# Kernel optimization log

Hardware: AMD Instinct MI355X
Metric: run time of the kernel (lower is better)

## Reference

```python
import jax, jax.numpy as jnp
import numpy as np

B, S, F_IN, D, H, DFF, L = 64, 256, 64, 512, 8, 2048, 6
A_DIM, FEAT, OUT = 8, 32, 5
EPS = 1e-3  # keras default epsilon for BatchNorm/LayerNorm


def _sinusoidal_pes(seq_len, d_model):
    pos = np.arange(seq_len)[:, None].astype(np.float32)
    i = np.arange(d_model)[None, :].astype(np.float32)
    angle = pos / np.power(10000.0, (2.0 * np.floor(i / 2.0)) / d_model)
    pe = np.zeros((seq_len, d_model), dtype=np.float32)
    pe[:, 0::2] = np.sin(angle[:, 0::2])
    pe[:, 1::2] = np.cos(angle[:, 1::2])
    return jnp.asarray(pe)


def setup_inputs() -> dict:
    key = jax.random.key(0)
    ks = jax.random.split(key, 16)
    w = lambda k, shape: 0.02 * jax.random.normal(k, shape, dtype=jnp.float32)
    return {
        'state': jax.random.normal(ks[0], (B, S, F_IN), dtype=jnp.float32),
        'action': jax.random.normal(ks[1], (B, A_DIM), dtype=jnp.float32),
        'pes': _sinusoidal_pes(S, D),
        'W_emb': w(ks[2], (F_IN, D)), 'b_emb': jnp.zeros((D,), jnp.float32),
        'Wq': w(ks[3], (L, D, D)), 'bq': jnp.zeros((L, D), jnp.float32),
        'Wk': w(ks[4], (L, D, D)), 'bk': jnp.zeros((L, D), jnp.float32),
        'Wv': w(ks[5], (L, D, D)), 'bv': jnp.zeros((L, D), jnp.float32),
        'Wo': w(ks[6], (L, D, D)), 'bo': jnp.zeros((L, D), jnp.float32),
        'bn_gamma': jnp.ones((L, D), jnp.float32), 'bn_beta': jnp.zeros((L, D), jnp.float32),
        'W1': w(ks[7], (L, D, DFF)), 'b1': jnp.zeros((L, DFF), jnp.float32),
        'W2': w(ks[8], (L, DFF, D)), 'b2': jnp.zeros((L, D), jnp.float32),
        'ln_gamma': jnp.ones((L, D), jnp.float32), 'ln_beta': jnp.zeros((L, D), jnp.float32),
        'Wf': w(ks[9], (S * D, FEAT)), 'bf': jnp.zeros((FEAT,), jnp.float32),
        'Wfin': w(ks[10], (FEAT + A_DIM, OUT)), 'bfin': jnp.zeros((OUT,), jnp.float32),
    }


def _encoder(x, pes, layer_params):
    # x: [B, S, D]
    x = x + pes  # positional encoding

    def step(h, p):
        Wq, bq, Wk, bk, Wv, bv, Wo, bo, gb, bb, W1, b1, W2, b2, gl, bl = p
        b, s, d = h.shape
        dh = d // H
        q = (h @ Wq + bq).reshape(b, s, H, dh)
        k = (h @ Wk + bk).reshape(b, s, H, dh)
        v = (h @ Wv + bv).reshape(b, s, H, dh)
        scores = jnp.einsum('bqhd,bkhd->bhqk', q, k) / jnp.sqrt(jnp.asarray(dh, h.dtype))
        attn = jax.nn.softmax(scores, axis=-1)
        ctx = jnp.einsum('bhqk,bkhd->bqhd', attn, v).reshape(b, s, d)
        ctx = ctx @ Wo + bo
        y = h + ctx
        # BatchNormalization over (batch, seq), per-channel (training-mode batch stats)
        mu = y.mean(axis=(0, 1))
        var = y.var(axis=(0, 1))
        y = gb * (y - mu) * jax.lax.rsqrt(var + EPS) + bb
        # FFN + residual + LayerNorm
        f = jax.nn.relu(y @ W1 + b1) @ W2 + b2
        z = y + f
        mu2 = z.mean(axis=-1, keepdims=True)
        var2 = z.var(axis=-1, keepdims=True)
        z = gl * (z - mu2) * jax.lax.rsqrt(var2 + EPS) + bl
        return z, None

    x, _ = jax.lax.scan(step, x, layer_params)
    return x


def reference(state, action, pes, W_emb, b_emb, Wq, bq, Wk, bk, Wv, bv, Wo, bo,
              bn_gamma, bn_beta, W1, b1, W2, b2, ln_gamma, ln_beta, Wf, bf, Wfin, bfin):
    x = state @ W_emb + b_emb                       # [B, S, D]
    layer_params = (Wq, bq, Wk, bk, Wv, bv, Wo, bo, bn_gamma, bn_beta,
                    W1, b1, W2, b2, ln_gamma, ln_beta)
    enc = _encoder(x, pes, layer_params)            # [B, S, D]
    flat = enc.reshape(enc.shape[0], -1)            # [B, S*D]
    feat = flat @ Wf + bf                           # [B, 32]
    out = jnp.concatenate([feat, action], axis=-1) @ Wfin + bfin  # [B, 5]
    return out
```

## Files before the change

kernel.cpp:

```cpp
#include <hip/hip_runtime.h>

typedef short bf16x8 __attribute__((ext_vector_type(8)));
typedef float f32x4 __attribute__((ext_vector_type(4)));
typedef unsigned short us;

#define BN_EPS 1e-3f

static __device__ __forceinline__ us f2bs(float x) {
  unsigned int u = __builtin_bit_cast(unsigned int, x);
  unsigned int r = (u + 0x7FFFu + ((u >> 16) & 1u)) >> 16;
  return (us)r;
}
static __device__ __forceinline__ float b2f(us v) {
  unsigned int u = (unsigned int)v << 16;
  return __builtin_bit_cast(float, u);
}

static __device__ __forceinline__ void gl_lds16(const us* g, us* l) {
  __builtin_amdgcn_global_load_lds(
      (const __attribute__((address_space(1))) void*)g,
      (__attribute__((address_space(3))) void*)l, 16, 0, 0);
}

__global__ __launch_bounds__(256) void transpose_bf16(
    const float* __restrict__ src, us* __restrict__ dst, int K, int N,
    long sstride, long dstride) {
  long sbs = (long)blockIdx.z * sstride;
  long sbd = (long)blockIdx.z * dstride;
  __shared__ float tile[32][33];
  int tx = threadIdx.x & 31, ty = threadIdx.x >> 5;
  int k0 = blockIdx.x * 32, n0 = blockIdx.y * 32;
  for (int i = 0; i < 32; i += 8)
    tile[ty + i][tx] = src[sbs + (long)(k0 + ty + i) * N + n0 + tx];
  __syncthreads();
  for (int i = 0; i < 32; i += 8)
    dst[sbd + (long)(n0 + ty + i) * K + k0 + tx] = f2bs(tile[tx][ty + i]);
}

__global__ __launch_bounds__(256) void embed_kernel(
    const float* __restrict__ state, const float* __restrict__ Wemb,
    const float* __restrict__ bemb, const float* __restrict__ pes,
    us* __restrict__ hb) {
  int t = threadIdx.x;
  int row0 = blockIdx.x * 8;
  __shared__ float st[8][64];
  {
    int i = t;
    st[i >> 6][i & 63] = state[(long)row0 * 64 + i];
    i += 256;
    st[i >> 6][i & 63] = state[(long)row0 * 64 + i];
  }
  __syncthreads();
  int c0 = t, c1 = t + 256;
  float acc0[8], acc1[8];
#pragma unroll
  for (int r = 0; r < 8; ++r) { acc0[r] = 0.f; acc1[r] = 0.f; }
  for (int kk = 0; kk < 64; ++kk) {
    float w0 = Wemb[kk * 512 + c0], w1 = Wemb[kk * 512 + c1];
#pragma unroll
    for (int r = 0; r < 8; ++r) {
      acc0[r] += st[r][kk] * w0;
      acc1[r] += st[r][kk] * w1;
    }
  }
  float be0 = bemb[c0], be1 = bemb[c1];
#pragma unroll
  for (int r = 0; r < 8; ++r) {
    int row = row0 + r, s = row & 255;
    hb[(long)row * 512 + c0] = f2bs(acc0[r] + be0 + pes[(long)s * 512 + c0]);
    hb[(long)row * 512 + c1] = f2bs(acc1[r] + be1 + pes[(long)s * 512 + c1]);
  }
}

enum { EPI_QKV = 0, EPI_RESID_BF16 = 1, EPI_RELU_BF16 = 2, EPI_FFN2_F32 = 3,
       EPI_FEAT = 4 };

template <int BM, int BN, int WM, int WN, int EPI>
__global__ __launch_bounds__((BM / WM) * (BN / WN) * 64)
void gemm_bt(const us* __restrict__ A, int lda, long batchA,
             const us* __restrict__ Bt, int ldb, long batchB,
             void* __restrict__ Cout, void* __restrict__ C2,
             void* __restrict__ C3, int ldc,
             const float* __restrict__ bias,
             const us* __restrict__ resid,
             const float* __restrict__ gsum, const float* __restrict__ gsumsq,
             const float* __restrict__ gamma, const float* __restrict__ beta,
             int K) {
  constexpr int WCols = BN / WN;
  constexpr int NT = (BM / WM) * (BN / WN) * 64;
  constexpr int NW = NT / 64;
  constexpr int MI = WM / 16, NI = WN / 16;
  constexpr int LA = BM / 8;
  constexpr int LB = BN / 8;
  const int tid = threadIdx.x;
  const int w = tid >> 6, l = tid & 63;
  const int wr = w / WCols, wc = w % WCols;
  const int lr = l & 15, lh = l >> 4;
  const int z = blockIdx.z;
  const long m0 = (long)blockIdx.x * BM;
  const long n0 = (long)blockIdx.y * BN;
  A += (long)z * batchA;
  Bt += (long)z * batchB;
  __shared__ __align__(16) us smem[BM * 64 + BN * 64];
  us* Asm = smem;
  us* Bsm = smem + BM * 64;
  const int srow = l >> 3, scol = (l & 7) << 3;
  f32x4 acc[MI][NI] = {};
  for (int kt = 0; kt < K; kt += 64) {
    __syncthreads();
    for (int j = w; j < LA; j += NW) {
      int rb = j * 8;
      gl_lds16(A + (m0 + rb + srow) * lda + kt + scol, Asm + rb * 64);
    }
    for (int j = w; j < LB; j += NW) {
      int rb = j * 8;
      gl_lds16(Bt + (n0 + rb + srow) * ldb + kt + scol, Bsm + rb * 64);
    }
    asm volatile("s_waitcnt vmcnt(0)" ::: "memory");
    __syncthreads();
#pragma unroll
    for (int kk = 0; kk < 64; kk += 32) {
      bf16x8 af[MI], bfr[NI];
#pragma unroll
      for (int mi = 0; mi < MI; ++mi)
        af[mi] = *(const bf16x8*)&Asm[(wr * WM + mi * 16 + lr) * 64 + kk + lh * 8];
#pragma unroll
      for (int ni = 0; ni < NI; ++ni)
        bfr[ni] = *(const bf16x8*)&Bsm[(wc * WN + ni * 16 + lr) * 64 + kk + lh * 8];
#pragma unroll
      for (int mi = 0; mi < MI; ++mi)
#pragma unroll
        for (int ni = 0; ni < NI; ++ni)
          acc[mi][ni] = __builtin_amdgcn_mfma_f32_16x16x32_bf16(
              af[mi], bfr[ni], acc[mi][ni], 0, 0, 0);
    }
  }

  if constexpr (EPI == EPI_QKV) {
    const int seg = (int)(n0 >> 9);
    const int nc0 = (int)(n0 & 511);
    if (seg == 2) {
#pragma unroll
      for (int mi = 0; mi < MI; ++mi) {
#pragma unroll
        for (int ni = 0; ni < NI; ++ni) {
          const int segc = nc0 + wc * WN + ni * 16 + lr;
          const float bv_ = beta[segc];
          ushort4 pv;
#pragma unroll
          for (int q_ = 0; q_ < 4; ++q_)
            ((us*)&pv)[q_] = f2bs(acc[mi][ni][q_] + bv_);
          const long row0g = m0 + wr * WM + mi * 16 + lh * 4;
          const long o = (((row0g >> 8) * 8 + (segc >> 6)) * 64 + (segc & 63)) *
                             256 + (row0g & 255);
          *(ushort4*)&((us*)C3)[o] = pv;
        }
      }
    } else {
      __syncthreads();
#pragma unroll
      for (int mi = 0; mi < MI; ++mi)
#pragma unroll
        for (int ni = 0; ni < NI; ++ni) {
          const int cl = wc * WN + ni * 16 + lr;
          const float bv_ = seg == 0 ? bias[nc0 + cl] : gamma[nc0 + cl];
#pragma unroll
          for (int q_ = 0; q_ < 4; ++q_) {
            const int rl = wr * WM + mi * 16 + lh * 4 + q_;
            smem[rl * BN + cl] = f2bs(acc[mi][ni][q_] + bv_);
          }
        }
      __syncthreads();
      us* dstp = seg == 0 ? (us*)Cout : (us*)C2;
      for (int i = tid; i < (BM * BN) / 8; i += NT) {
        const int idx = i * 8;
        const int row = idx / BN, colc = idx % BN;
        *(uint4*)&dstp[(m0 + row) * 512 + nc0 + colc] = *(uint4*)&smem[idx];
      }
    }
  } else if constexpr ((EPI == EPI_RELU_BF16 || EPI == EPI_RESID_BF16) &&
                       BM == 128 && BN == 128) {
    __syncthreads();
#pragma unroll
    for (int mi = 0; mi < MI; ++mi)
#pragma unroll
      for (int ni = 0; ni < NI; ++ni) {
        const int cl = wc * WN + ni * 16 + lr;
        const float bv_ = bias[(int)n0 + cl];
#pragma unroll
        for (int q_ = 0; q_ < 4; ++q_) {
          const int rl = wr * WM + mi * 16 + lh * 4 + q_;
          float v = acc[mi][ni][q_] + bv_;
          if constexpr (EPI == EPI_RELU_BF16) {
            smem[rl * BN + cl] = f2bs(fmaxf(v, 0.f));
          } else {
            v += b2f(resid[(m0 + rl) * ldc + (int)n0 + cl]);
            smem[rl * BN + cl] = f2bs(v);
          }
        }
      }
    __syncthreads();
    for (int i = tid; i < (BM * BN) / 8; i += NT) {
      const int idx = i * 8;
      const int row = idx / BN, colc = idx % BN;
      *(uint4*)&((us*)Cout)[(m0 + row) * ldc + n0 + colc] = *(uint4*)&smem[idx];
    }
  } else {
#pragma unroll
    for (int mi = 0; mi < MI; ++mi) {
#pragma unroll
      for (int ni = 0; ni < NI; ++ni) {
        const int col = (int)n0 + wc * WN + ni * 16 + lr;
        float bv_ = 0.f;
        if constexpr (EPI != EPI_FEAT) bv_ = bias[col];
        float aa = 0.f, bb2 = 0.f;
        if constexpr (EPI == EPI_FFN2_F32) {
          const float invN = 1.f / 16384.f;
          float mu = gsum[col] * invN;
          float var = gsumsq[col] * invN - mu * mu;
          aa = gamma[col] * rsqrtf(var + BN_EPS);
          bb2 = beta[col] - mu * aa;
        }
#pragma unroll
        for (int q_ = 0; q_ < 4; ++q_) {
          const long row = m0 + wr * WM + mi * 16 + lh * 4 + q_;
          float v = acc[mi][ni][q_] + bv_;
          if constexpr (EPI == EPI_FEAT) {
            atomicAdd(&((float*)Cout)[row * ldc + col], v);
          } else if constexpr (EPI == EPI_FFN2_F32) {
            float ybn = b2f(resid[row * ldc + col]) * aa + bb2;
            ((float*)Cout)[row * ldc + col] = ybn + v;
          }
        }
      }
    }
  }
}

__global__ __launch_bounds__(256) void attn_kernel(
    const us* __restrict__ q, const us* __restrict__ k,
    const us* __restrict__ vt, us* __restrict__ ctx) {
  const int half = blockIdx.x;
  const int z = blockIdx.y;
  const int b = z >> 3, hh = z & 7;
  const long qkBase = (long)b * 131072 + hh * 64;
  const int tid = threadIdx.x, w = tid >> 6, l = tid & 63;
  const int lr = l & 15, lh = l >> 4;
  __shared__ __align__(16) us Qs[32][72];
  __shared__ __align__(16) us Ks[64][72];
  __shared__ __align__(16) us Pb[32][264];
  __shared__ float fred[32][2];
  const int qr = (w >> 1) * 16, qc = (w & 1) * 32;
  const us* vb = vt + (long)z * 16384;
  const int ldr = tid >> 3, ldc = (tid & 7) << 3;

  for (int qi = 0; qi < 4; ++qi) {
    const int qb = half * 4 + qi;
    *(uint4*)&Qs[ldr][ldc] =
        *(const uint4*)(q + qkBase + (long)(qb * 32 + ldr) * 512 + ldc);
    f32x4 sacc[4][2] = {};
    for (int skb = 0; skb < 4; ++skb) {
      __syncthreads();
      for (int i = tid; i < 512; i += 256) {
        int r = i >> 3, c = (i & 7) << 3;
        *(uint4*)&Ks[r][c] =
            *(const uint4*)(k + qkBase + (long)(skb * 64 + r) * 512 + c);
      }
      __syncthreads();
#pragma unroll
      for (int kh = 0; kh < 2; ++kh) {
        bf16x8 aq = *(const bf16x8*)&Qs[qr + lr][kh * 32 + lh * 8];
#pragma unroll
        for (int ni = 0; ni < 2; ++ni) {
          bf16x8 bkk = *(const bf16x8*)&Ks[qc + ni * 16 + lr][kh * 32 + lh * 8];
          sacc[skb][ni] = __builtin_amdgcn_mfma_f32_16x16x32_bf16(
              aq, bkk, sacc[skb][ni], 0, 0, 0);
        }
      }
    }
    float m0[4] = {-1e30f, -1e30f, -1e30f, -1e30f};
#pragma unroll
    for (int skb = 0; skb < 4; ++skb)
#pragma unroll
      for (int ni = 0; ni < 2; ++ni)
#pragma unroll
        for (int q_ = 0; q_ < 4; ++q_) {
          float v = sacc[skb][ni][q_] * 0.125f;
          sacc[skb][ni][q_] = v;
          m0[q_] = fmaxf(m0[q_], v);
        }
#pragma unroll
    for (int off = 1; off < 16; off <<= 1)
#pragma unroll
      for (int q_ = 0; q_ < 4; ++q_)
        m0[q_] = fmaxf(m0[q_], __shfl_xor(m0[q_], off));
    if (lr == 0) {
#pragma unroll
      for (int q_ = 0; q_ < 4; ++q_) fred[qr + lh * 4 + q_][w & 1] = m0[q_];
    }
    __syncthreads();
#pragma unroll
    for (int q_ = 0; q_ < 4; ++q_) {
      int row = qr + lh * 4 + q_;
      m0[q_] = fmaxf(fred[row][0], fred[row][1]);
    }
    float s0[4] = {0.f, 0.f, 0.f, 0.f};
#pragma unroll
    for (int skb = 0; skb < 4; ++skb)
#pragma unroll
      for (int ni = 0; ni < 2; ++ni)
#pragma unroll
        for (int q_ = 0; q_ < 4; ++q_) {
          float e = __expf(sacc[skb][ni][q_] - m0[q_]);
          sacc[skb][ni][q_] = e;
          s0[q_] += e;
        }
#pragma unroll
    for (int off = 1; off < 16; off <<= 1)
#pragma unroll
      for (int q_ = 0; q_ < 4; ++q_) s0[q_] += __shfl_xor(s0[q_], off);
    __syncthreads();
    if (lr == 0) {
#pragma unroll
      for (int q_ = 0; q_ < 4; ++q_) fred[qr + lh * 4 + q_][w & 1] = s0[q_];
    }
    __syncthreads();
#pragma unroll
    for (int q_ = 0; q_ < 4; ++q_) {
      int row = qr + lh * 4 + q_;
      s0[q_] = 1.f / (fred[row][0] + fred[row][1]);
    }
#pragma unroll
    for (int skb = 0; skb < 4; ++skb)
#pragma unroll
      for (int ni = 0; ni < 2; ++ni)
#pragma unroll
        for (int q_ = 0; q_ < 4; ++q_)
          Pb[qr + lh * 4 + q_][skb * 64 + qc + ni * 16 + lr] =
              f2bs(sacc[skb][ni][q_] * s0[q_]);
    f32x4 pacc[2] = {};
    for (int kc = 0; kc < 256; kc += 64) {
      __syncthreads();
      for (int i = tid; i < 512; i += 256) {
        int r = i >> 3, c = (i & 7) << 3;
        *(uint4*)&Ks[r][c] = *(const uint4*)(vb + (long)r * 256 + kc + c);
      }
      __syncthreads();
#pragma unroll
      for (int kh = 0; kh < 2; ++kh) {
        bf16x8 ap = *(const bf16x8*)&Pb[qr + lr][kc + kh * 32 + lh * 8];
#pragma unroll
        for (int ni = 0; ni < 2; ++ni) {
          bf16x8 bv2 = *(const bf16x8*)&Ks[qc + ni * 16 + lr][kh * 32 + lh * 8];
          pacc[ni] = __builtin_amdgcn_mfma_f32_16x16x32_bf16(
              ap, bv2, pacc[ni], 0, 0, 0);
        }
      }
    }
    const long cb2 = ((long)(b * 256 + qb * 32)) * 512 + hh * 64;
#pragma unroll
    for (int ni = 0; ni < 2; ++ni)
#pragma unroll
      for (int q_ = 0; q_ < 4; ++q_) {
        int row = qr + lh * 4 + q_;
        int col = qc + ni * 16 + lr;
        ctx[cb2 + (long)row * 512 + col] = f2bs(pacc[ni][q_]);
      }
  }
}

__global__ __launch_bounds__(256) void bn_stats(const us* __restrict__ y,
                                                float* __restrict__ gsum,
                                                float* __restrict__ gsumsq) {
  int t = threadIdx.x;
  long base = (long)blockIdx.x * 64 * 512;
  float s0 = 0, q0 = 0, s1 = 0, q1 = 0;
  for (int r = 0; r < 64; ++r) {
    ushort2 v = *(const ushort2*)(y + base + r * 512 + 2 * t);
    float v0 = b2f(v.x), v1 = b2f(v.y);
    s0 += v0; q0 += v0 * v0;
    s1 += v1; q1 += v1 * v1;
  }
  atomicAdd(&gsum[2 * t], s0);
  atomicAdd(&gsumsq[2 * t], q0);
  atomicAdd(&gsum[2 * t + 1], s1);
  atomicAdd(&gsumsq[2 * t + 1], q1);
}

__global__ __launch_bounds__(256) void bn_apply(
    const us* __restrict__ y, const float* __restrict__ gsum,
    const float* __restrict__ gsumsq, const float* __restrict__ gamma,
    const float* __restrict__ beta, us* __restrict__ ybb) {
  long e = ((long)blockIdx.x * 256 + threadIdx.x) * 4;
  int c = (int)(e & 511);
  const float invN = 1.f / 16384.f;
  ushort4 v = *(const ushort4*)(y + e);
  ushort4 r;
#pragma unroll
  for (int j = 0; j < 4; ++j) {
    int cj = c + j;
    float mu = gsum[cj] * invN;
    float var = gsumsq[cj] * invN - mu * mu;
    float a = gamma[cj] * rsqrtf(var + BN_EPS);
    float b = beta[cj] - mu * a;
    ((us*)&r)[j] = f2bs(b2f(((us*)&v)[j]) * a + b);
  }
  *(ushort4*)(ybb + e) = r;
}

__global__ __launch_bounds__(128) void ln_kernel(
    const float* __restrict__ zin, const float* __restrict__ g,
    const float* __restrict__ b, us* __restrict__ hb) {
  int r = blockIdx.x, t = threadIdx.x;
  const float* zr = zin + (long)r * 512;
  float4 v = *(const float4*)(zr + t * 4);
  float s = v.x + v.y + v.z + v.w;
  float qs = v.x * v.x + v.y * v.y + v.z * v.z + v.w * v.w;
  for (int off = 32; off >= 1; off >>= 1) {
    s += __shfl_down(s, off);
    qs += __shfl_down(qs, off);
  }
  __shared__ float ls[2], lq[2];
  if ((t & 63) == 0) {
    ls[t >> 6] = s;
    lq[t >> 6] = qs;
  }
  __syncthreads();
  float mu = (ls[0] + ls[1]) * (1.f / 512.f);
  float var = (lq[0] + lq[1]) * (1.f / 512.f) - mu * mu;
  float rs = rsqrtf(var + BN_EPS);
  float4 gg = *(const float4*)(g + t * 4);
  float4 bb = *(const float4*)(b + t * 4);
  ushort4 hv;
  ((us*)&hv)[0] = f2bs(gg.x * (v.x - mu) * rs + bb.x);
  ((us*)&hv)[1] = f2bs(gg.y * (v.y - mu) * rs + bb.y);
  ((us*)&hv)[2] = f2bs(gg.z * (v.z - mu) * rs + bb.z);
  ((us*)&hv)[3] = f2bs(gg.w * (v.w - mu) * rs + bb.w);
  *(ushort4*)(hb + (long)r * 512 + t * 4) = hv;
}

__global__ void zerof(float* __restrict__ p, int n) {
  int i = blockIdx.x * 256 + threadIdx.x;
  if (i < n) p[i] = 0.f;
}

__global__ __launch_bounds__(320) void final_head(
    const float* __restrict__ feat, const float* __restrict__ bf_,
    const float* __restrict__ action, const float* __restrict__ Wfin,
    const float* __restrict__ bfin, float* __restrict__ out) {
  int t = threadIdx.x;
  int b = t & 63, o = t >> 6;
  float acc = bfin[o];
  for (int j = 0; j < 32; ++j) acc += (feat[b * 32 + j] + bf_[j]) * Wfin[j * 5 + o];
  for (int j = 0; j < 8; ++j) acc += action[b * 8 + j] * Wfin[(32 + j) * 5 + o];
  out[b * 5 + o] = acc;
}

extern "C" void kernel_launch(void* const* d_in, const int* in_sizes, int n_in,
                              void* d_out, int out_size, void* d_ws,
                              size_t ws_size, hipStream_t stream) {
  const float* state = (const float*)d_in[0];
  const float* action = (const float*)d_in[1];
  const float* pes = (const float*)d_in[2];
  const float* W_emb = (const float*)d_in[3];
  const float* b_emb = (const float*)d_in[4];
  const float* Wq = (const float*)d_in[5];
  const float* bq = (const float*)d_in[6];
  const float* Wk = (const float*)d_in[7];
  const float* bk = (const float*)d_in[8];
  const float* Wv = (const float*)d_in[9];
  const float* bv = (const float*)d_in[10];
  const float* Wo = (const float*)d_in[11];
  const float* bo = (const float*)d_in[12];
  const float* bn_g = (const float*)d_in[13];
  const float* bn_b = (const float*)d_in[14];
  const float* W1 = (const float*)d_in[15];
  const float* b1 = (const float*)d_in[16];
  const float* W2 = (const float*)d_in[17];
  const float* b2 = (const float*)d_in[18];
  const float* ln_g = (const float*)d_in[19];
  const float* ln_b = (const float*)d_in[20];
  const float* Wf = (const float*)d_in[21];
  const float* bf_ = (const float*)d_in[22];
  const float* Wfin = (const float*)d_in[23];
  const float* bfin = (const float*)d_in[24];
  float* out = (float*)d_out;
  (void)in_sizes; (void)n_in; (void)out_size;

  char* wp = (char*)d_ws;
  size_t off = 0;
  auto take = [&](size_t bytes) {
    void* p = wp + off;
    off += (bytes + 255) & ~(size_t)255;
    return p;
  };
  us* qkvT = (us*)take(6ull * 1536 * 512 * 2);
  us* WoT = (us*)take(6ull * 512 * 512 * 2);
  us* W1T = (us*)take(6ull * 2048 * 512 * 2);
  us* W2T = (us*)take(6ull * 512 * 2048 * 2);
  us* WfT = (us*)take(32ull * 131072 * 2);
  us* hb = (us*)take(16384ull * 512 * 2);
  us* ybf = (us*)take(16384ull * 512 * 2);
  us* qb_ = (us*)take(16384ull * 512 * 2);
  us* kb_ = (us*)take(16384ull * 512 * 2);
  us* vt = (us*)take(16384ull * 512 * 2);
  us* bigR4 = (us*)take(33554432ull * 2);
  float* gsum = (float*)take(512 * 4);
  float* gsumsq = (float*)take(512 * 4);
  float* feat = (float*)take(2048 * 4);
  us* ctxb = bigR4;
  us* f1 = bigR4;
  us* ybb = kb_;
  float* zb = (float*)qb_;

  if (off > ws_size) return;

  transpose_bf16<<<dim3(16, 16, 6), 256, 0, stream>>>(Wq, qkvT, 512, 512,
                                                      262144, 786432);
  transpose_bf16<<<dim3(16, 16, 6), 256, 0, stream>>>(Wk, qkvT + 262144, 512,
                                                      512, 262144, 786432);
  transpose_bf16<<<dim3(16, 16, 6), 256, 0, stream>>>(Wv, qkvT + 524288, 512,
                                                      512, 262144, 786432);
  transpose_bf16<<<dim3(16, 16, 6), 256, 0, stream>>>(Wo, WoT, 512, 512,
                                                      262144, 262144);
  transpose_bf16<<<dim3(16, 64, 6), 256, 0, stream>>>(W1, W1T, 512, 2048,
                                                      1048576, 1048576);
  transpose_bf16<<<dim3(64, 16, 6), 256, 0, stream>>>(W2, W2T, 2048, 512,
                                                      1048576, 1048576);
  transpose_bf16<<<dim3(4096, 1, 1), 256, 0, stream>>>(Wf, WfT, 131072, 32,
                                                       0, 0);
  embed_kernel<<<2048, 256, 0, stream>>>(state, W_emb, b_emb, pes, hb);

  for (int l = 0; l < 6; ++l) {
    const us* qkvTl = qkvT + (size_t)l * 786432;
    const us* WoTl = WoT + (size_t)l * 262144;
    const us* W1Tl = W1T + (size_t)l * 1048576;
    const us* W2Tl = W2T + (size_t)l * 1048576;

    gemm_bt<128, 128, 64, 64, EPI_QKV><<<dim3(128, 12, 1), 256, 0, stream>>>(
        hb, 512, 0, qkvTl, 512, 0, qb_, kb_, vt, 512, bq + l * 512,
        nullptr, nullptr, nullptr, bk + l * 512, bv + l * 512, 512);
    attn_kernel<<<dim3(2, 512), 256, 0, stream>>>(qb_, kb_, vt, ctxb);
    gemm_bt<128, 128, 64, 64, EPI_RESID_BF16><<<dim3(128, 4, 1), 256, 0, stream>>>(
        ctxb, 512, 0, WoTl, 512, 0, ybf, nullptr, nullptr, 512, bo + l * 512,
        hb, nullptr, nullptr, nullptr, nullptr, 512);
    zerof<<<4, 256, 0, stream>>>(gsum, 1024);
    bn_stats<<<256, 256, 0, stream>>>(ybf, gsum, gsumsq);
    bn_apply<<<8192, 256, 0, stream>>>(ybf, gsum, gsumsq, bn_g + l * 512,
                                       bn_b + l * 512, ybb);
    gemm_bt<128, 128, 64, 64, EPI_RELU_BF16><<<dim3(128, 16, 1), 256, 0, stream>>>(
        ybb, 512, 0, W1Tl, 512, 0, f1, nullptr, nullptr, 2048, b1 + l * 2048,
        nullptr, nullptr, nullptr, nullptr, nullptr, 512);
    gemm_bt<128, 128, 64, 64, EPI_FFN2_F32><<<dim3(128, 4, 1), 256, 0, stream>>>(
        f1, 2048, 0, W2Tl, 2048, 0, zb, nullptr, nullptr, 512, b2 + l * 512,
        ybf, gsum, gsumsq, bn_g + l * 512, bn_b + l * 512, 2048);
    ln_kernel<<<16384, 128, 0, stream>>>(zb, ln_g + l * 512, ln_b + l * 512, hb);
  }

  zerof<<<8, 256, 0, stream>>>(feat, 2048);
  gemm_bt<64, 32, 32, 16, EPI_FEAT><<<dim3(1, 1, 128), 256, 0, stream>>>(
      hb, 131072, 1024, WfT, 131072, 1024, feat, nullptr, nullptr, 32,
      nullptr, nullptr, nullptr, nullptr, nullptr, nullptr, 1024);
  final_head<<<1, 320, 0, stream>>>(feat, bf_, action, Wfin, bfin, out);
}
```

Before: 1.634 ms.

## Fold batchnorm affine into W1 weights and store FFN2 output as bf16

Removes the per-element bn_apply pass. The BatchNorm scale and shift are computed once per channel, and the scale is folded into a scaled copy of W1 with the shift folded into the W1 bias, so the FFN1 GEMM consumes the raw residual output directly. The FFN2 epilogue now applies the BN affine with precomputed coefficients and writes bf16 through the shared-memory staged path instead of fp32, and the LayerNorm reads bf16. This cuts a full read/write pass over the activation and halves the FFN2 output traffic. It adds a small weight-folding kernel per layer and extra bf16 rounding of the scaled weights and the pre-LN sum.

```diff
diff --git a/kernel.cpp b/kernel.cpp
--- a/kernel.cpp
+++ b/kernel.cpp
@@ -72,7 +72,7 @@
   }
 }
 
-enum { EPI_QKV = 0, EPI_RESID_BF16 = 1, EPI_RELU_BF16 = 2, EPI_FFN2_F32 = 3,
+enum { EPI_QKV = 0, EPI_RESID_BF16 = 1, EPI_RELU_BF16 = 2, EPI_FFN2_BF16 = 3,
        EPI_FEAT = 4 };
 
 template <int BM, int BN, int WM, int WN, int EPI>
@@ -178,24 +178,33 @@
         *(uint4*)&dstp[(m0 + row) * 512 + nc0 + colc] = *(uint4*)&smem[idx];
       }
     }
-  } else if constexpr ((EPI == EPI_RELU_BF16 || EPI == EPI_RESID_BF16) &&
-                       BM == 128 && BN == 128) {
+  } else if constexpr ((EPI == EPI_RELU_BF16 || EPI == EPI_RESID_BF16 ||
+                        EPI == EPI_FFN2_BF16) && BM == 128 && BN == 128) {
     __syncthreads();
 #pragma unroll
     for (int mi = 0; mi < MI; ++mi)
 #pragma unroll
       for (int ni = 0; ni < NI; ++ni) {
         const int cl = wc * WN + ni * 16 + lr;
-        const float bv_ = bias[(int)n0 + cl];
+        const int col = (int)n0 + cl;
+        const float bv_ = bias[col];
+        float aa = 0.f, bb2 = 0.f;
+        if constexpr (EPI == EPI_FFN2_BF16) {
+          aa = gsum[col];
+          bb2 = gsumsq[col];
+        }
 #pragma unroll
         for (int q_ = 0; q_ < 4; ++q_) {
           const int rl = wr * WM + mi * 16 + lh * 4 + q_;
           float v = acc[mi][ni][q_] + bv_;
           if constexpr (EPI == EPI_RELU_BF16) {
             smem[rl * BN + cl] = f2bs(fmaxf(v, 0.f));
+          } else if constexpr (EPI == EPI_RESID_BF16) {
+            v += b2f(resid[(m0 + rl) * ldc + col]);
+            smem[rl * BN + cl] = f2bs(v);
           } else {
-            v += b2f(resid[(m0 + rl) * ldc + (int)n0 + cl]);
-            smem[rl * BN + cl] = f2bs(v);
+            float ybn = b2f(resid[(m0 + rl) * ldc + col]) * aa + bb2;
+            smem[rl * BN + cl] = f2bs(ybn + v);
           }
         }
       }
@@ -211,25 +220,11 @@
 #pragma unroll
       for (int ni = 0; ni < NI; ++ni) {
         const int col = (int)n0 + wc * WN + ni * 16 + lr;
-        float bv_ = 0.f;
-        if constexpr (EPI != EPI_FEAT) bv_ = bias[col];
-        float aa = 0.f, bb2 = 0.f;
-        if constexpr (EPI == EPI_FFN2_F32) {
-          const float invN = 1.f / 16384.f;
-          float mu = gsum[col] * invN;
-          float var = gsumsq[col] * invN - mu * mu;
-          aa = gamma[col] * rsqrtf(var + BN_EPS);
-          bb2 = beta[col] - mu * aa;
-        }
 #pragma unroll
         for (int q_ = 0; q_ < 4; ++q_) {
           const long row = m0 + wr * WM + mi * 16 + lh * 4 + q_;
-          float v = acc[mi][ni][q_] + bv_;
           if constexpr (EPI == EPI_FEAT) {
-            atomicAdd(&((float*)Cout)[row * ldc + col], v);
-          } else if constexpr (EPI == EPI_FFN2_F32) {
-            float ybn = b2f(resid[row * ldc + col]) * aa + bb2;
-            ((float*)Cout)[row * ldc + col] = ybn + v;
+            atomicAdd(&((float*)Cout)[row * ldc + col], acc[mi][ni][q_]);
           }
         }
       }
@@ -387,35 +382,53 @@
   atomicAdd(&gsumsq[2 * t + 1], q1);
 }
 
-__global__ __launch_bounds__(256) void bn_apply(
-    const us* __restrict__ y, const float* __restrict__ gsum,
-    const float* __restrict__ gsumsq, const float* __restrict__ gamma,
-    const float* __restrict__ beta, us* __restrict__ ybb) {
-  long e = ((long)blockIdx.x * 256 + threadIdx.x) * 4;
-  int c = (int)(e & 511);
-  const float invN = 1.f / 16384.f;
-  ushort4 v = *(const ushort4*)(y + e);
-  ushort4 r;
-#pragma unroll
-  for (int j = 0; j < 4; ++j) {
-    int cj = c + j;
-    float mu = gsum[cj] * invN;
-    float var = gsumsq[cj] * invN - mu * mu;
-    float a = gamma[cj] * rsqrtf(var + BN_EPS);
-    float b = beta[cj] - mu * a;
-    ((us*)&r)[j] = f2bs(b2f(((us*)&v)[j]) * a + b);
-  }
-  *(ushort4*)(ybb + e) = r;
+__global__ void bn_coef(float* __restrict__ gsum, float* __restrict__ gsumsq,
+                        const float* __restrict__ gamma,
+                        const float* __restrict__ beta) {
+  int c = blockIdx.x * 256 + threadIdx.x;
+  if (c < 512) {
+    const float invN = 1.f / 16384.f;
+    float mu = gsum[c] * invN;
+    float var = gsumsq[c] * invN - mu * mu;
+    float a = gamma[c] * rsqrtf(var + BN_EPS);
+    float b = beta[c] - mu * a;
+    gsum[c] = a;
+    gsumsq[c] = b;
+  }
+}
+
+__global__ __launch_bounds__(256) void fold_w1(
+    const us* __restrict__ W1T, const float* __restrict__ aa,
+    const float* __restrict__ bb, const float* __restrict__ b1,
+    us* __restrict__ W1s, float* __restrict__ bias1f) {
+  int n = blockIdx.x * 4 + (threadIdx.x >> 6);
+  int l = threadIdx.x & 63;
+  int k0 = l * 8;
+  const us* row = W1T + (long)n * 512;
+  us tmp[8], outv[8];
+  *(uint4*)tmp = *(const uint4*)(row + k0);
+  float dot = 0.f;
+#pragma unroll
+  for (int j = 0; j < 8; ++j) {
+    float wv = b2f(tmp[j]);
+    dot += bb[k0 + j] * wv;
+    outv[j] = f2bs(aa[k0 + j] * wv);
+  }
+  *(uint4*)(W1s + (long)n * 512 + k0) = *(uint4*)outv;
+  for (int off = 32; off >= 1; off >>= 1) dot += __shfl_down(dot, off);
+  if (l == 0) bias1f[n] = b1[n] + dot;
 }
 
 __global__ __launch_bounds__(128) void ln_kernel(
-    const float* __restrict__ zin, const float* __restrict__ g,
+    const us* __restrict__ zin, const float* __restrict__ g,
     const float* __restrict__ b, us* __restrict__ hb) {
   int r = blockIdx.x, t = threadIdx.x;
-  const float* zr = zin + (long)r * 512;
-  float4 v = *(const float4*)(zr + t * 4);
-  float s = v.x + v.y + v.z + v.w;
-  float qs = v.x * v.x + v.y * v.y + v.z * v.z + v.w * v.w;
+  const us* zr = zin + (long)r * 512;
+  ushort4 vz = *(const ushort4*)(zr + t * 4);
+  float v0 = b2f(((us*)&vz)[0]), v1 = b2f(((us*)&vz)[1]);
+  float v2 = b2f(((us*)&vz)[2]), v3 = b2f(((us*)&vz)[3]);
+  float s = v0 + v1 + v2 + v3;
+  float qs = v0 * v0 + v1 * v1 + v2 * v2 + v3 * v3;
   for (int off = 32; off >= 1; off >>= 1) {
     s += __shfl_down(s, off);
     qs += __shfl_down(qs, off);
@@ -432,10 +445,10 @@
   float4 gg = *(const float4*)(g + t * 4);
   float4 bb = *(const float4*)(b + t * 4);
   ushort4 hv;
-  ((us*)&hv)[0] = f2bs(gg.x * (v.x - mu) * rs + bb.x);
-  ((us*)&hv)[1] = f2bs(gg.y * (v.y - mu) * rs + bb.y);
-  ((us*)&hv)[2] = f2bs(gg.z * (v.z - mu) * rs + bb.z);
-  ((us*)&hv)[3] = f2bs(gg.w * (v.w - mu) * rs + bb.w);
+  ((us*)&hv)[0] = f2bs(gg.x * (v0 - mu) * rs + bb.x);
+  ((us*)&hv)[1] = f2bs(gg.y * (v1 - mu) * rs + bb.y);
+  ((us*)&hv)[2] = f2bs(gg.z * (v2 - mu) * rs + bb.z);
+  ((us*)&hv)[3] = f2bs(gg.w * (v3 - mu) * rs + bb.w);
   *(ushort4*)(hb + (long)r * 512 + t * 4) = hv;
 }
 
@@ -501,6 +514,8 @@
   us* WfT = (us*)take(32ull * 131072 * 2);
   us* hb = (us*)take(16384ull * 512 * 2);
   us* ybf = (us*)take(16384ull * 512 * 2);
+  us* W1s = (us*)take(2048ull * 512 * 2);
+  float* bias1f = (float*)take(2048 * 4);
   us* qb_ = (us*)take(16384ull * 512 * 2);
   us* kb_ = (us*)take(16384ull * 512 * 2);
   us* vt = (us*)take(16384ull * 512 * 2);
@@ -510,8 +525,7 @@
   float* feat = (float*)take(2048 * 4);
   us* ctxb = bigR4;
   us* f1 = bigR4;
-  us* ybb = kb_;
-  float* zb = (float*)qb_;
+  us* zbf = qb_;
 
   if (off > ws_size) return;
 
@@ -546,15 +560,18 @@
         hb, nullptr, nullptr, nullptr, nullptr, 512);
     zerof<<<4, 256, 0, stream>>>(gsum, 1024);
     bn_stats<<<256, 256, 0, stream>>>(ybf, gsum, gsumsq);
-    bn_apply<<<8192, 256, 0, stream>>>(ybf, gsum, gsumsq, bn_g + l * 512,
-                                       bn_b + l * 512, ybb);
+    bn_coef<<<2, 256, 0, stream>>>(gsum, gsumsq, bn_g + l * 512,
+                                   bn_b + l * 512);
+    fold_w1<<<512, 256, 0, stream>>>(W1Tl, gsum, gsumsq, b1 + l * 2048, W1s,
+                                     bias1f);
     gemm_bt<128, 128, 64, 64, EPI_RELU_BF16><<<dim3(128, 16, 1), 256, 0, stream>>>(
-        ybb, 512, 0, W1Tl, 512, 0, f1, nullptr, nullptr, 2048, b1 + l * 2048,
+        ybf, 512, 0, W1s, 512, 0, f1, nullptr, nullptr, 2048, bias1f,
         nullptr, nullptr, nullptr, nullptr, nullptr, 512);
-    gemm_bt<128, 128, 64, 64, EPI_FFN2_F32><<<dim3(128, 4, 1), 256, 0, stream>>>(
-        f1, 2048, 0, W2Tl, 2048, 0, zb, nullptr, nullptr, 512, b2 + l * 512,
-        ybf, gsum, gsumsq, bn_g + l * 512, bn_b + l * 512, 2048);
-    ln_kernel<<<16384, 128, 0, stream>>>(zb, ln_g + l * 512, ln_b + l * 512, hb);
+    gemm_bt<128, 128, 64, 64, EPI_FFN2_BF16><<<dim3(128, 4, 1), 256, 0, stream>>>(
+        f1, 2048, 0, W2Tl, 2048, 0, zbf, nullptr, nullptr, 512, b2 + l * 512,
+        ybf, gsum, gsumsq, nullptr, nullptr, 2048);
+    ln_kernel<<<16384, 128, 0, stream>>>(zbf, ln_g + l * 512, ln_b + l * 512,
+                                         hb);
   }
 
   zerof<<<8, 256, 0, stream>>>(feat, 2048);
```

New measurement: 1.596 ms. -2.3%, faster.
